# Kernel tuning notes

Hardware: AMD Instinct MI355X
Metric: run time of the kernel (lower is better)

The kernel has to match this reference:

```python
import jax, jax.numpy as jnp
import numpy as np

OVERFLOW_MARGIN = 1e-08
N, BBN_DIM, CBN_DIM = 8192, 32, 512


def setup_inputs() -> dict:
    key = jax.random.key(0)
    k1, k2, k3 = jax.random.split(key, 3)
    bbn = jax.random.uniform(k1, (N, BBN_DIM), dtype=jnp.float32)
    cbn = jax.random.normal(k2, (N, CBN_DIM), dtype=jnp.float32)
    # Dense(cbn_dim) params: glorot-ish init
    W = jax.random.normal(k3, (CBN_DIM, CBN_DIM), dtype=jnp.float32) / np.sqrt(CBN_DIM)
    b = jnp.zeros((CBN_DIM,), dtype=jnp.float32)
    return {"bbn": bbn, "cbn": cbn, "W": W, "b": b}


def reference(bbn, cbn, W, b):
    # --- build_adjacency_hamming(bbn): soft hamming-similarity adjacency [N,N] ---
    code_length = jnp.asarray(bbn.shape[1], dtype=bbn.dtype)
    m1 = bbn - 1.0
    c1 = bbn @ m1.T          # [N,N]
    c2 = m1 @ bbn.T          # [N,N]
    normalized_dist = jnp.abs(c1 + c2) / code_length
    adj = jnp.power(1.0 - normalized_dist, 1.4)

    # --- graph laplacian: D^{-1/2} A D^{-1/2} (broadcast form of eye*d_inv_sqrt matmuls) ---
    d = jnp.sum(adj, axis=1)                      # row sums == adj @ ones
    d_inv_sqrt = jnp.power(d + OVERFLOW_MARGIN, -0.5)
    laplacian = d_inv_sqrt[:, None] * adj * d_inv_sqrt[None, :]

    # --- GCN spectral conv: L @ Dense(cbn), then sigmoid ---
    fc_sc = cbn @ W + b                           # [N, cbn_dim]
    conv_sc = laplacian @ fc_sc                   # [N, cbn_dim]
    return jax.nn.sigmoid(conv_sc)
```

## Files before the change

### kernel.cpp

```cpp
#include <hip/hip_runtime.h>

#define NROWS 8192
#define BBND  32
#define CBND  512
#define JQ    4096
#define NR    64
#define ABUFB 8192

typedef unsigned short u16;
typedef unsigned int   u32;
typedef __bf16 bf16x8 __attribute__((ext_vector_type(8)));
typedef float  f32x4  __attribute__((ext_vector_type(4)));
typedef float  f32x16 __attribute__((ext_vector_type(16)));
typedef u32    u32x4  __attribute__((ext_vector_type(4)));
typedef u32    u32x2  __attribute__((ext_vector_type(2)));

#define ZERO4  (f32x4){0.f,0.f,0.f,0.f}
#define ZERO16 (f32x16){0.f,0.f,0.f,0.f,0.f,0.f,0.f,0.f,0.f,0.f,0.f,0.f,0.f,0.f,0.f,0.f}

#define BAR asm volatile("s_waitcnt lgkmcnt(0)\n\ts_barrier" ::: "memory")

static __device__ inline u16 f2bf(float f) {
    unsigned u = __builtin_bit_cast(unsigned, f);
    unsigned r = (u + 0x7FFFu + ((u >> 16) & 1u)) >> 16;
    return (u16)r;
}

static __device__ inline float pow14(float base) {
    return __builtin_amdgcn_exp2f(1.4f * __builtin_amdgcn_logf(base));
}

static __device__ inline float adj_eval(float dot, float sij) {
    float x = fabsf(2.f * dot - sij);
    float base = fmaxf(1.f - x * (1.f / 32.f), 0.f);
    return pow14(base);
}

static __device__ inline float sigmoidf_fast(float v) {
    float e = __builtin_amdgcn_exp2f(-1.44269504f * v);
    return 1.f / (1.f + e);
}

static __device__ inline u32 cvtpk(float a, float b) {
    u32 r;
    asm("v_cvt_pk_bf16_f32 %0, %1, %2" : "=v"(r) : "v"(a), "v"(b));
    return r;
}

static __device__ inline f32x4 MFMA16(bf16x8 a, bf16x8 b, f32x4 c) {
    return __builtin_amdgcn_mfma_f32_16x16x32_bf16(a, b, c, 0, 0, 0);
}
static __device__ inline f32x16 MFMA32(bf16x8 a, bf16x8 b, f32x16 c) {
    return __builtin_amdgcn_mfma_f32_32x32x16_bf16(a, b, c, 0, 0, 0);
}

__global__ __launch_bounds__(512) void k_prep(const float* __restrict__ bbn,
                                              const float* __restrict__ W,
                                              float* __restrict__ s,
                                              u16* __restrict__ bbn_bf,
                                              u16* __restrict__ WT) {
    int idx = blockIdx.x * 512 + threadIdx.x;
    int c = idx >> 9, k = idx & 511;
    WT[idx] = f2bf(W[k * CBND + c]);
    if (idx < NROWS) {
        const f32x4* row = reinterpret_cast<const f32x4*>(bbn + idx * BBND);
        float sum = 0.f;
        u16* dst = bbn_bf + idx * BBND;
#pragma unroll
        for (int q = 0; q < 8; ++q) {
            f32x4 v = row[q];
#pragma unroll
            for (int e = 0; e < 4; ++e) {
                sum += v[e];
                dst[q * 4 + e] = f2bf(v[e]);
            }
        }
        s[idx] = sum;
    }
}

__global__ __launch_bounds__(1024) void k_deg(const u16* __restrict__ bbn_bf,
                                              const float* __restrict__ s,
                                              float* __restrict__ dinv) {
    __shared__ float part[16][16];
    int ibase = blockIdx.x * 16;
    int tid = threadIdx.x;
    int w = tid >> 6, l = tid & 63, lg = l >> 4, lr = l & 15;

    bf16x8 afrag = *reinterpret_cast<const bf16x8*>(bbn_bf + (ibase + lr) * BBND + lg * 8);
    float si[4];
#pragma unroll
    for (int r = 0; r < 4; ++r) si[r] = s[ibase + lg * 4 + r];

    float dacc[4] = {0.f, 0.f, 0.f, 0.f};
    int j0 = w * (NROWS / 16);
    bf16x8 nbf = *reinterpret_cast<const bf16x8*>(bbn_bf + (j0 + lr) * BBND + lg * 8);
    float nsj = s[j0 + lr];
    for (int jt = 0; jt < NROWS / 16; jt += 16) {
        bf16x8 bfrag = nbf;
        float sj = nsj;
        if (jt + 16 < NROWS / 16) {
            int jn = j0 + jt + 16;
            nbf = *reinterpret_cast<const bf16x8*>(bbn_bf + (jn + lr) * BBND + lg * 8);
            nsj = s[jn + lr];
        }
        f32x4 dot = MFMA16(afrag, bfrag, ZERO4);
#pragma unroll
        for (int r = 0; r < 4; ++r) dacc[r] += adj_eval(dot[r], si[r] + sj);
    }
#pragma unroll
    for (int off = 1; off < 16; off <<= 1)
#pragma unroll
        for (int r = 0; r < 4; ++r) dacc[r] += __shfl_xor(dacc[r], off, 64);

    if (lr == 0) {
#pragma unroll
        for (int r = 0; r < 4; ++r) part[w][lg * 4 + r] = dacc[r];
    }
    __syncthreads();
    if (tid < 16) {
        float d = 0.f;
#pragma unroll
        for (int q = 0; q < 16; ++q) d += part[q][tid];
        dinv[ibase + tid] = rsqrtf(d + 1e-8f);
    }
}

__global__ __launch_bounds__(512) void k_fc(const float* __restrict__ cbn,
                                            const u16* __restrict__ WT,
                                            const float* __restrict__ bvec,
                                            const float* __restrict__ dinv,
                                            u16* __restrict__ g_blk) {
    __shared__ __align__(16) u16 Clds[64 * 512];
    int bx = blockIdx.x;
    int ch = bx & 1;
    int jcol = (bx >> 1) * 64;
    int tid = threadIdx.x;
    int w = tid >> 6, l = tid & 63, lg = l >> 4, lr = l & 15;
    int wq = w & 3, jh = w >> 2;

    char* Cl = (char*)&Clds[0];

#pragma unroll
    for (int p = 0; p < 8; ++p) {
        int gidx = p * 512 + tid;
        int row = gidx >> 6, sl = gidx & 63;
        const f32x4* src = reinterpret_cast<const f32x4*>(cbn + (jcol + row) * CBND + sl * 8);
        f32x4 v0 = src[0], v1 = src[1];
        bf16x8 bv;
#pragma unroll
        for (int e = 0; e < 4; ++e) { bv[e] = (__bf16)v0[e]; bv[e + 4] = (__bf16)v1[e]; }
        *reinterpret_cast<bf16x8*>(Cl + row * 1024 + ((sl ^ (row & 7)) << 4)) = bv;
    }
    __syncthreads();

    int r7 = lr & 7;
    for (int q = 0; q < 4; ++q) {
        int cb = ch * 4 + q;
        int crow = cb * 64 + wq * 16;
        f32x4 acc0 = ZERO4, acc1 = ZERO4;
        for (int k0 = 0; k0 < CBND; k0 += 32) {
            bf16x8 afrag = *reinterpret_cast<const bf16x8*>(WT + (crow + lr) * CBND + k0 + lg * 8);
            int slot = (k0 >> 3) + lg;
            int row0 = jh * 32 + lr;
            bf16x8 b0 = *reinterpret_cast<const bf16x8*>(Cl + row0 * 1024 + ((slot ^ r7) << 4));
            bf16x8 b1 = *reinterpret_cast<const bf16x8*>(Cl + (row0 + 16) * 1024 + ((slot ^ r7) << 4));
            acc0 = MFMA16(afrag, b0, acc0);
            acc1 = MFMA16(afrag, b1, acc1);
        }
#pragma unroll
        for (int f = 0; f < 2; ++f) {
            f32x4 af = f ? acc1 : acc0;
#pragma unroll
            for (int r = 0; r < 4; ++r) {
                int c = crow + lg * 4 + r;
                int j = jcol + jh * 32 + f * 16 + lr;
                float val = af[r] + bvec[c];
                g_blk[(((j >> 3) * 512 + c) << 3) + (j & 7)] = f2bf(val * dinv[j]);
            }
        }
    }
}

#define LOADB(T, R) { \
    const char* p = gB + (long)(T) * 65536; \
    R##0 = *reinterpret_cast<const u32x4*>(p); \
    R##1 = *reinterpret_cast<const u32x4*>(p + 16384); \
    R##2 = *reinterpret_cast<const u32x4*>(p + 32768); \
    R##3 = *reinterpret_cast<const u32x4*>(p + 49152); \
}

#define LOADG(ST) { \
    int jg = jbase + (ST) * 64 + jq8 * 16; \
    gJ = *reinterpret_cast<const bf16x8*>(bbn_bf + (jg + lr) * BBND + lg * 8); \
    gS = *reinterpret_cast<const f32x4*>(s + jg + lg * 4); \
}

#define GENP(WB) { \
    f32x4 dot = MFMA16(gJ, fragI, ZERO4); \
    u32 p0 = cvtpk(adj_eval(dot[0], si + gS[0]), adj_eval(dot[1], si + gS[1])); \
    u32 p1 = cvtpk(adj_eval(dot[2], si + gS[2]), adj_eval(dot[3], si + gS[3])); \
    *reinterpret_cast<u32x2*>(Ab + (WB) * ABUFB + gw) = (u32x2){p0, p1}; \
}

#define CONVP(RB, R) { \
    const char* Ar = Ab + (RB) * ABUFB; \
    bf16x8 t0l = *reinterpret_cast<const bf16x8*>(Ar + a0); \
    bf16x8 t0h = *reinterpret_cast<const bf16x8*>(Ar + a0 + 4096); \
    c00 = MFMA32(t0l, __builtin_bit_cast(bf16x8, R##0), c00); \
    c10 = MFMA32(t0h, __builtin_bit_cast(bf16x8, R##0), c10); \
    bf16x8 t1l = *reinterpret_cast<const bf16x8*>(Ar + a1); \
    bf16x8 t1h = *reinterpret_cast<const bf16x8*>(Ar + a1 + 4096); \
    c00 = MFMA32(t1l, __builtin_bit_cast(bf16x8, R##1), c00); \
    c10 = MFMA32(t1h, __builtin_bit_cast(bf16x8, R##1), c10); \
    bf16x8 t2l = *reinterpret_cast<const bf16x8*>(Ar + a2); \
    bf16x8 t2h = *reinterpret_cast<const bf16x8*>(Ar + a2 + 4096); \
    c00 = MFMA32(t2l, __builtin_bit_cast(bf16x8, R##2), c00); \
    c10 = MFMA32(t2h, __builtin_bit_cast(bf16x8, R##2), c10); \
    bf16x8 t3l = *reinterpret_cast<const bf16x8*>(Ar + a3); \
    bf16x8 t3h = *reinterpret_cast<const bf16x8*>(Ar + a3 + 4096); \
    c00 = MFMA32(t3l, __builtin_bit_cast(bf16x8, R##3), c00); \
    c10 = MFMA32(t3h, __builtin_bit_cast(bf16x8, R##3), c10); \
}

#define EPI(ACC, IH) { \
    _Pragma("unroll") \
    for (int reg = 0; reg < 16; ++reg) { \
        int rowD = (reg & 3) + 8 * (reg >> 2) + 4 * lh; \
        Pq[(long)(ibase + (IH) * 32 + rowD) * CBND + w * 32 + l31] = ACC[reg]; \
    } \
}

__global__ __launch_bounds__(1024, 4) void k_conv(const u16* __restrict__ bbn_bf,
                                                  const float* __restrict__ s,
                                                  const u16* __restrict__ g_blk,
                                                  float* __restrict__ P) {
    __shared__ __align__(16) u16 Alds[2][64 * 64];

    int bx = blockIdx.x;
    int jq = bx & 1;
    int it = bx >> 1;
    int ibase = it * 64;
    int jbase = jq * JQ;

    int tid = threadIdx.x;
    int w = tid >> 6, l = tid & 63;
    int lr = l & 15, lg = l >> 4, l31 = l & 31, lh = l >> 5;
    int iq = w & 3, jq8 = w >> 2;

    bf16x8 fragI = *reinterpret_cast<const bf16x8*>(bbn_bf + (ibase + iq * 16 + lr) * BBND + lg * 8);
    float si = s[ibase + iq * 16 + lr];

    char* Ab = (char*)&Alds[0][0];
    float* Pq = P + (long)jq * (NROWS * CBND);

    const char* gB = (const char*)g_blk + (long)jbase * 1024 + lh * 8192
                   + (w * 32 + l31) * 16;

    int r7 = l31 & 7;
    int abase = l31 * 128;
    int a0 = abase + (((0 + lh) ^ r7) << 4);
    int a1 = abase + (((2 + lh) ^ r7) << 4);
    int a2 = abase + (((4 + lh) ^ r7) << 4);
    int a3 = abase + (((6 + lh) ^ r7) << 4);

    int grow = iq * 16 + lr;
    int gw = grow * 128 + (((jq8 * 2 + (lg >> 1)) ^ (grow & 7)) << 4) + (lg & 1) * 8;

    f32x16 c00 = ZERO16, c10 = ZERO16;

    u32x4 rA0, rA1, rA2, rA3;
    u32x4 rB0, rB1, rB2, rB3;
    bf16x8 gJ;
    f32x4 gS;

    LOADG(0);
    GENP(0);
    LOADG(1);
    LOADB(0, rA);
    BAR;

    for (int st2 = 0; st2 < NR; st2 += 2) {
        LOADB(st2 + 1, rB);
        GENP(1);
        if (st2 + 2 < NR) LOADG(st2 + 2);
        CONVP(0, rA);
        BAR;
        int tn = (st2 + 2 < NR) ? st2 + 2 : NR - 1;
        LOADB(tn, rA);
        if (st2 + 2 < NR) {
            GENP(0);
            if (st2 + 3 < NR) LOADG(st2 + 3);
        }
        CONVP(1, rB);
        BAR;
    }

    EPI(c00, 0);
    EPI(c10, 1);
}

__global__ __launch_bounds__(256) void k_comb(const float* __restrict__ dinv,
                                              const float* __restrict__ P,
                                              float* __restrict__ out) {
    int idx = blockIdx.x * 256 + threadIdx.x;
    float di = dinv[idx >> 7];
    f32x4 a = *reinterpret_cast<const f32x4*>(P + (long)idx * 4);
    f32x4 b = *reinterpret_cast<const f32x4*>(P + (long)NROWS * CBND + (long)idx * 4);
    f32x4 v;
#pragma unroll
    for (int e = 0; e < 4; ++e) v[e] = sigmoidf_fast((a[e] + b[e]) * di);
    *reinterpret_cast<f32x4*>(out + (long)idx * 4) = v;
}

extern "C" void kernel_launch(void* const* d_in, const int* in_sizes, int n_in,
                              void* d_out, int out_size, void* d_ws, size_t ws_size,
                              hipStream_t stream) {
    const float* bbn = (const float*)d_in[0];
    const float* cbn = (const float*)d_in[1];
    const float* W   = (const float*)d_in[2];
    const float* b   = (const float*)d_in[3];
    float* out = (float*)d_out;

    char* ws = (char*)d_ws;
    float* s      = (float*)ws;  ws += NROWS * 4;
    float* dinv   = (float*)ws;  ws += NROWS * 4;
    u16* bbn_bf   = (u16*)ws;    ws += NROWS * BBND * 2;
    u16* WT       = (u16*)ws;    ws += CBND * CBND * 2;
    u16* g_blk    = (u16*)ws;    ws += (size_t)CBND * NROWS * 2;
    float* P      = (float*)ws;  ws += (size_t)2 * NROWS * CBND * 4;

    k_prep<<<512, 512, 0, stream>>>(bbn, W, s, bbn_bf, WT);
    k_deg<<<NROWS / 16, 1024, 0, stream>>>(bbn_bf, s, dinv);
    k_fc<<<(NROWS / 64) * 2, 512, 0, stream>>>(cbn, WT, b, dinv, g_blk);
    k_conv<<<(NROWS / 64) * 2, 1024, 0, stream>>>(bbn_bf, s, g_blk, P);
    k_comb<<<(NROWS * CBND / 4) / 256, 256, 0, stream>>>(dinv, P, out);
}
```

Before: 146.3 us.

## Run degree and FC kernels concurrently in one launch, apply column scaling in conv

Merges the degree computation and the Dense layer into one kernel whose first 512 blocks compute dinv and remaining 256 blocks compute fc. This removes a launch and lets the two independent phases overlap. To break the dependency, the right-hand dinv scaling moves from the fc output into the conv kernel's adjacency tile generation, which adds a dinv load and four multiplies per tile. It also slightly changes the bf16 rounding point of the scaling.

```diff
diff --git a/kernel.cpp b/kernel.cpp
--- a/kernel.cpp
+++ b/kernel.cpp
@@ -79,108 +79,108 @@
     }
 }
 
-__global__ __launch_bounds__(1024) void k_deg(const u16* __restrict__ bbn_bf,
-                                              const float* __restrict__ s,
-                                              float* __restrict__ dinv) {
-    __shared__ float part[16][16];
-    int ibase = blockIdx.x * 16;
+__global__ __launch_bounds__(1024, 4) void k_degfc(const u16* __restrict__ bbn_bf,
+                                                   const float* __restrict__ s,
+                                                   float* __restrict__ dinv,
+                                                   const float* __restrict__ cbn,
+                                                   const u16* __restrict__ WT,
+                                                   const float* __restrict__ bvec,
+                                                   u16* __restrict__ g_blk) {
+    __shared__ __align__(16) u16 Clds[64 * 512];
+    int bx = blockIdx.x;
     int tid = threadIdx.x;
     int w = tid >> 6, l = tid & 63, lg = l >> 4, lr = l & 15;
 
-    bf16x8 afrag = *reinterpret_cast<const bf16x8*>(bbn_bf + (ibase + lr) * BBND + lg * 8);
-    float si[4];
-#pragma unroll
-    for (int r = 0; r < 4; ++r) si[r] = s[ibase + lg * 4 + r];
-
-    float dacc[4] = {0.f, 0.f, 0.f, 0.f};
-    int j0 = w * (NROWS / 16);
-    bf16x8 nbf = *reinterpret_cast<const bf16x8*>(bbn_bf + (j0 + lr) * BBND + lg * 8);
-    float nsj = s[j0 + lr];
-    for (int jt = 0; jt < NROWS / 16; jt += 16) {
-        bf16x8 bfrag = nbf;
-        float sj = nsj;
-        if (jt + 16 < NROWS / 16) {
-            int jn = j0 + jt + 16;
-            nbf = *reinterpret_cast<const bf16x8*>(bbn_bf + (jn + lr) * BBND + lg * 8);
-            nsj = s[jn + lr];
-        }
-        f32x4 dot = MFMA16(afrag, bfrag, ZERO4);
-#pragma unroll
-        for (int r = 0; r < 4; ++r) dacc[r] += adj_eval(dot[r], si[r] + sj);
+    if (bx < 512) {
+        float (*part)[16] = reinterpret_cast<float(*)[16]>(&Clds[0]);
+        int ibase = bx * 16;
+
+        bf16x8 afrag = *reinterpret_cast<const bf16x8*>(bbn_bf + (ibase + lr) * BBND + lg * 8);
+        float si[4];
+#pragma unroll
+        for (int r = 0; r < 4; ++r) si[r] = s[ibase + lg * 4 + r];
+
+        float dacc[4] = {0.f, 0.f, 0.f, 0.f};
+        int j0 = w * (NROWS / 16);
+        bf16x8 nbf = *reinterpret_cast<const bf16x8*>(bbn_bf + (j0 + lr) * BBND + lg * 8);
+        float nsj = s[j0 + lr];
+        for (int jt = 0; jt < NROWS / 16; jt += 16) {
+            bf16x8 bfrag = nbf;
+            float sj = nsj;
+            if (jt + 16 < NROWS / 16) {
+                int jn = j0 + jt + 16;
+                nbf = *reinterpret_cast<const bf16x8*>(bbn_bf + (jn + lr) * BBND + lg * 8);
+                nsj = s[jn + lr];
+            }
+            f32x4 dot = MFMA16(afrag, bfrag, ZERO4);
+#pragma unroll
+            for (int r = 0; r < 4; ++r) dacc[r] += adj_eval(dot[r], si[r] + sj);
+        }
+#pragma unroll
+        for (int off = 1; off < 16; off <<= 1)
+#pragma unroll
+            for (int r = 0; r < 4; ++r) dacc[r] += __shfl_xor(dacc[r], off, 64);
+
+        if (lr == 0) {
+#pragma unroll
+            for (int r = 0; r < 4; ++r) part[w][lg * 4 + r] = dacc[r];
+        }
+        __syncthreads();
+        if (tid < 16) {
+            float d = 0.f;
+#pragma unroll
+            for (int q = 0; q < 16; ++q) d += part[q][tid];
+            dinv[ibase + tid] = rsqrtf(d + 1e-8f);
+        }
+    } else {
+        char* Cl = (char*)&Clds[0];
+        int fb = bx - 512;
+        int ch = fb & 1;
+        int jcol = (fb >> 1) * 64;
+
+#pragma unroll
+        for (int p = 0; p < 4; ++p) {
+            int gidx = p * 1024 + tid;
+            int row = gidx >> 6, sl = gidx & 63;
+            const f32x4* src = reinterpret_cast<const f32x4*>(cbn + (jcol + row) * CBND + sl * 8);
+            f32x4 v0 = src[0], v1 = src[1];
+            bf16x8 bv;
+#pragma unroll
+            for (int e = 0; e < 4; ++e) { bv[e] = (__bf16)v0[e]; bv[e + 4] = (__bf16)v1[e]; }
+            *reinterpret_cast<bf16x8*>(Cl + row * 1024 + ((sl ^ (row & 7)) << 4)) = bv;
+        }
+        __syncthreads();
+
+        int wq = w & 3, jh = (w >> 2) & 1, qh = w >> 3;
+        int r7 = lr & 7;
+#pragma unroll
+        for (int qq = 0; qq < 2; ++qq) {
+            int cb = ch * 4 + qh * 2 + qq;
+            int crow = cb * 64 + wq * 16;
+            f32x4 acc0 = ZERO4, acc1 = ZERO4;
+            for (int k0 = 0; k0 < CBND; k0 += 32) {
+                bf16x8 afrag = *reinterpret_cast<const bf16x8*>(WT + (crow + lr) * CBND + k0 + lg * 8);
+                int slot = (k0 >> 3) + lg;
+                int row0 = jh * 32 + lr;
+                bf16x8 b0 = *reinterpret_cast<const bf16x8*>(Cl + row0 * 1024 + ((slot ^ r7) << 4));
+                bf16x8 b1 = *reinterpret_cast<const bf16x8*>(Cl + (row0 + 16) * 1024 + ((slot ^ r7) << 4));
+                acc0 = MFMA16(afrag, b0, acc0);
+                acc1 = MFMA16(afrag, b1, acc1);
+            }
+#pragma unroll
+            for (int f = 0; f < 2; ++f) {
+                f32x4 af = f ? acc1 : acc0;
+#pragma unroll
+                for (int r = 0; r < 4; ++r) {
+                    int c = crow + lg * 4 + r;
+                    int j = jcol + jh * 32 + f * 16 + lr;
+                    g_blk[(((j >> 3) * 512 + c) << 3) + (j & 7)] = f2bf(af[r] + bvec[c]);
+                }
+            }
+        }
     }
-#pragma unroll
-    for (int off = 1; off < 16; off <<= 1)
-#pragma unroll
-        for (int r = 0; r < 4; ++r) dacc[r] += __shfl_xor(dacc[r], off, 64);
-
-    if (lr == 0) {
-#pragma unroll
-        for (int r = 0; r < 4; ++r) part[w][lg * 4 + r] = dacc[r];
-    }
-    __syncthreads();
-    if (tid < 16) {
-        float d = 0.f;
-#pragma unroll
-        for (int q = 0; q < 16; ++q) d += part[q][tid];
-        dinv[ibase + tid] = rsqrtf(d + 1e-8f);
-    }
-}
-
-__global__ __launch_bounds__(512) void k_fc(const float* __restrict__ cbn,
-                                            const u16* __restrict__ WT,
-                                            const float* __restrict__ bvec,
-                                            const float* __restrict__ dinv,
-                                            u16* __restrict__ g_blk) {
-    __shared__ __align__(16) u16 Clds[64 * 512];
-    int bx = blockIdx.x;
-    int ch = bx & 1;
-    int jcol = (bx >> 1) * 64;
-    int tid = threadIdx.x;
-    int w = tid >> 6, l = tid & 63, lg = l >> 4, lr = l & 15;
-    int wq = w & 3, jh = w >> 2;
-
-    char* Cl = (char*)&Clds[0];
-
-#pragma unroll
-    for (int p = 0; p < 8; ++p) {
-        int gidx = p * 512 + tid;
-        int row = gidx >> 6, sl = gidx & 63;
-        const f32x4* src = reinterpret_cast<const f32x4*>(cbn + (jcol + row) * CBND + sl * 8);
-        f32x4 v0 = src[0], v1 = src[1];
-        bf16x8 bv;
-#pragma unroll
-        for (int e = 0; e < 4; ++e) { bv[e] = (__bf16)v0[e]; bv[e + 4] = (__bf16)v1[e]; }
-        *reinterpret_cast<bf16x8*>(Cl + row * 1024 + ((sl ^ (row & 7)) << 4)) = bv;
-    }
-    __syncthreads();
-
-    int r7 = lr & 7;
-    for (int q = 0; q < 4; ++q) {
-        int cb = ch * 4 + q;
-        int crow = cb * 64 + wq * 16;
-        f32x4 acc0 = ZERO4, acc1 = ZERO4;
-        for (int k0 = 0; k0 < CBND; k0 += 32) {
-            bf16x8 afrag = *reinterpret_cast<const bf16x8*>(WT + (crow + lr) * CBND + k0 + lg * 8);
-            int slot = (k0 >> 3) + lg;
-            int row0 = jh * 32 + lr;
-            bf16x8 b0 = *reinterpret_cast<const bf16x8*>(Cl + row0 * 1024 + ((slot ^ r7) << 4));
-            bf16x8 b1 = *reinterpret_cast<const bf16x8*>(Cl + (row0 + 16) * 1024 + ((slot ^ r7) << 4));
-            acc0 = MFMA16(afrag, b0, acc0);
-            acc1 = MFMA16(afrag, b1, acc1);
-        }
-#pragma unroll
-        for (int f = 0; f < 2; ++f) {
-            f32x4 af = f ? acc1 : acc0;
-#pragma unroll
-            for (int r = 0; r < 4; ++r) {
-                int c = crow + lg * 4 + r;
-                int j = jcol + jh * 32 + f * 16 + lr;
-                float val = af[r] + bvec[c];
-                g_blk[(((j >> 3) * 512 + c) << 3) + (j & 7)] = f2bf(val * dinv[j]);
-            }
-        }
-    }
-}
+}
+
 
 #define LOADB(T, R) { \
     const char* p = gB + (long)(T) * 65536; \
@@ -194,12 +194,13 @@
     int jg = jbase + (ST) * 64 + jq8 * 16; \
     gJ = *reinterpret_cast<const bf16x8*>(bbn_bf + (jg + lr) * BBND + lg * 8); \
     gS = *reinterpret_cast<const f32x4*>(s + jg + lg * 4); \
+    gD = *reinterpret_cast<const f32x4*>(dinv + jg + lg * 4); \
 }
 
 #define GENP(WB) { \
     f32x4 dot = MFMA16(gJ, fragI, ZERO4); \
-    u32 p0 = cvtpk(adj_eval(dot[0], si + gS[0]), adj_eval(dot[1], si + gS[1])); \
-    u32 p1 = cvtpk(adj_eval(dot[2], si + gS[2]), adj_eval(dot[3], si + gS[3])); \
+    u32 p0 = cvtpk(adj_eval(dot[0], si + gS[0]) * gD[0], adj_eval(dot[1], si + gS[1]) * gD[1]); \
+    u32 p1 = cvtpk(adj_eval(dot[2], si + gS[2]) * gD[2], adj_eval(dot[3], si + gS[3]) * gD[3]); \
     *reinterpret_cast<u32x2*>(Ab + (WB) * ABUFB + gw) = (u32x2){p0, p1}; \
 }
 
@@ -233,6 +234,7 @@
 
 __global__ __launch_bounds__(1024, 4) void k_conv(const u16* __restrict__ bbn_bf,
                                                   const float* __restrict__ s,
+                                                  const float* __restrict__ dinv,
                                                   const u16* __restrict__ g_blk,
                                                   float* __restrict__ P) {
     __shared__ __align__(16) u16 Alds[2][64 * 64];
@@ -272,7 +274,7 @@
     u32x4 rA0, rA1, rA2, rA3;
     u32x4 rB0, rB1, rB2, rB3;
     bf16x8 gJ;
-    f32x4 gS;
+    f32x4 gS, gD;
 
     LOADG(0);
     GENP(0);
@@ -331,8 +333,7 @@
     float* P      = (float*)ws;  ws += (size_t)2 * NROWS * CBND * 4;
 
     k_prep<<<512, 512, 0, stream>>>(bbn, W, s, bbn_bf, WT);
-    k_deg<<<NROWS / 16, 1024, 0, stream>>>(bbn_bf, s, dinv);
-    k_fc<<<(NROWS / 64) * 2, 512, 0, stream>>>(cbn, WT, b, dinv, g_blk);
-    k_conv<<<(NROWS / 64) * 2, 1024, 0, stream>>>(bbn_bf, s, g_blk, P);
+    k_degfc<<<768, 1024, 0, stream>>>(bbn_bf, s, dinv, cbn, WT, b, g_blk);
+    k_conv<<<(NROWS / 64) * 2, 1024, 0, stream>>>(bbn_bf, s, dinv, g_blk, P);
     k_comb<<<(NROWS * CBND / 4) / 256, 256, 0, stream>>>(dinv, P, out);
 }
```

Result: faster. 140.4 us (-4.0%).
